# Performance work log

Measured on AMD Instinct MI355X. Metric: run time of the kernel, lower is better.

Reference implementation:

```python
import jax, jax.numpy as jnp
import numpy as np
import itertools

SEQ, NF, K, SD, NB, NC, NOBJ = 8, 4, 3, 256, 512, 174, 10
BELTA, SUB, BATCH = 0.1, 10, 256
SCALES = list(range(NF, 0, -1))  # [4, 3, 2, 1]
D = (K + 1) * SD                 # per-frame fused feature dim = 1024


def _adjust_scales(seq_ind, is_test):
    # mirrors adjust_scale_train / adjust_scale_test
    scale_max = NF * 2
    if seq_ind < scale_max:
        return SCALES[-seq_ind:] if is_test else SCALES[-min(SUB, seq_ind):]
    return SCALES[:min(SUB, seq_ind) + 1]


def _plan(is_test):
    # Static (non-traced) relation-index plan: for each seq_ind, the set of
    # arithmetic-progression frame combinations selected by select_idx().
    plan = []
    for seq_ind in range(1, SEQ + 1):
        entries = []
        for scale in _adjust_scales(seq_ind, is_test):
            k = min(scale, seq_ind)
            division = seq_ind // scale
            sel = [r for r in itertools.combinations(range(seq_ind), k)
                   if np.all(np.diff(np.asarray(r)) == division)]
            if sel:
                entries.append((scale, np.asarray(sel, dtype=np.int32)))
        plan.append(entries)
    return plan


def _temporal_variation(init_input):
    # VLAD-style soft residuals. Source runs kmeans (non-deterministic,
    # numpy/detached); we use deterministic centers = first K points per clip
    # and reproduce the exact downstream math, including the (buggy but
    # faithful) scalar spectral-norm soft assignment shared by all points.
    x = init_input.reshape(-1, SEQ, NOBJ, SD)              # (B, S, O, d)
    flat = x.reshape(x.shape[0], SEQ * NOBJ, SD)           # (B, N, d)
    centers = flat[:, :K, :]                               # (B, K, d)
    diff = flat[:, None, :, :] - centers[:, :, None, :]    # (B, K, N, d)
    sig = jnp.linalg.svd(diff, compute_uv=False)[..., 0]   # matrix 2-norm per (b, k)
    w = jax.nn.softmax(-BELTA * sig ** 2, axis=-1)         # (B, K), same for every point
    # S[b,t,k,:] = sum_o w[b,k] * (x[b,t,o,:] - c[b,k,:])
    var = w[:, None, :, None] * (x.sum(axis=2)[:, :, None, :] - NOBJ * centers[:, None, :, :])
    return jax.lax.stop_gradient(var)  # source detaches via .detach().numpy()


def _fusion(x, w1, b1, w2, b2):
    # Sequential(ReLU, Linear, ReLU, Linear)
    h = jnp.maximum(jax.nn.relu(x) @ w1 + b1, 0.0)
    return h @ w2 + b2


def _forward(graph_out, init_input, params, is_test):
    B = graph_out.shape[0]
    var = _temporal_variation(init_input)                      # (B, S, K, d)
    new_input = jnp.concatenate([var.reshape(B, SEQ, K * SD), graph_out], axis=2)  # (B, S, D)
    rows = []
    for entries in _plan(bool(is_test)):
        acc = jnp.zeros((B, NC), graph_out.dtype)
        for scale, rel in entries:
            # batched gather of all sampled relations at once: (B, R, scale, D)
            g = new_input[:, rel, :].reshape(B, rel.shape[0], scale * D)
            acc = acc + _fusion(g, *params[scale]).sum(axis=1)
        rows.append(acc)
    return jnp.stack(rows, axis=1).reshape(B * SEQ, NC)


def setup_inputs():
    key = jax.random.key(0)
    ks = jax.random.split(key, 2 + 2 * len(SCALES))
    inp = {
        "graph_out": jax.random.normal(ks[0], (BATCH, SEQ, SD), jnp.float32),
        "init_input": jax.random.normal(ks[1], (BATCH * SEQ, NOBJ, SD), jnp.float32),
        "is_test": 0,
    }
    for i, s in enumerate(SCALES):
        inp[f"w1_{s}"] = jax.random.normal(ks[2 + 2 * i], (s * D, NB), jnp.float32) * 0.02
        inp[f"b1_{s}"] = jnp.zeros((NB,), jnp.float32)
        inp[f"w2_{s}"] = jax.random.normal(ks[3 + 2 * i], (NB, NC), jnp.float32) * 0.02
        inp[f"b2_{s}"] = jnp.zeros((NC,), jnp.float32)
    return inp


def reference(graph_out, init_input, is_test, w1_4, b1_4, w2_4, b2_4, w1_3, b1_3, w2_3, b2_3, w1_2, b1_2, w2_2, b2_2, w1_1, b1_1, w2_1, b2_1):
    params = {4: (w1_4, b1_4, w2_4, b2_4), 3: (w1_3, b1_3, w2_3, b2_3),
              2: (w1_2, b1_2, w2_2, b2_2), 1: (w1_1, b1_1, w2_1, b2_1)}
    return _forward(graph_out, init_input, params, is_test)
```

## Files before the change

kernel.cpp:

```cpp
#include <hip/hip_runtime.h>
#include <math.h>
#include <stdint.h>


typedef __attribute__((ext_vector_type(8))) short short8v;
typedef __attribute__((ext_vector_type(4))) short short4v;
typedef __attribute__((ext_vector_type(4))) float f32x4;

__device__ __forceinline__ short f2bf(float f) {
  uint32_t u = __float_as_uint(f);
  u += 0x7fffu + ((u >> 16) & 1u);
  return (short)(u >> 16);
}
__device__ __forceinline__ float bf2f(short s) {
  return __uint_as_float(((uint32_t)(uint16_t)s) << 16);
}
__device__ __forceinline__ void gload16(const void* g, void* l) {
  __builtin_amdgcn_global_load_lds(
      (const __attribute__((address_space(1))) void*)g,
      (__attribute__((address_space(3))) void*)l, 16, 0, 0);
}

__device__ const int8_t ROWS4[12][5] = {
  {3, 0,1,2,3},
  {4, 0,1,2,3},{4, 1,2,3,4},
  {5, 0,1,2,3},{5, 1,2,3,4},{5, 2,3,4,5},
  {6, 0,1,2,3},{6, 1,2,3,4},{6, 2,3,4,5},{6, 3,4,5,6},
  {7, 0,2,4,6},{7, 1,3,5,7},
};
__device__ const int8_t ROWS3[15][4] = {
  {2, 0,1,2},
  {3, 0,1,2},{3, 1,2,3},
  {4, 0,1,2},{4, 1,2,3},{4, 2,3,4},
  {5, 0,2,4},{5, 1,3,5},
  {6, 0,2,4},{6, 1,3,5},{6, 2,4,6},
  {7, 0,2,4},{7, 1,3,5},{7, 2,4,6},{7, 3,5,7},
};
__device__ const int8_t ROWS2[19][3] = {
  {1, 0,1},
  {2, 0,1},{2, 1,2},
  {3, 0,2},{3, 1,3},
  {4, 0,2},{4, 1,3},{4, 2,4},
  {5, 0,3},{5, 1,4},{5, 2,5},
  {6, 0,3},{6, 1,4},{6, 2,5},{6, 3,6},
  {7, 0,4},{7, 1,5},{7, 2,6},{7, 3,7},
};
__device__ const int8_t ROWS1[36][2] = {
  {0,0},
  {1,0},{1,1},
  {2,0},{2,1},{2,2},
  {3,0},{3,1},{3,2},{3,3},
  {4,0},{4,1},{4,2},{4,3},{4,4},
  {5,0},{5,1},{5,2},{5,3},{5,4},{5,5},
  {6,0},{6,1},{6,2},{6,3},{6,4},{6,5},{6,6},
  {7,0},{7,1},{7,2},{7,3},{7,4},{7,5},{7,6},{7,7},
};
__device__ const float CNT[8][4] = {
  {0,0,0,1},{0,0,1,2},{0,1,2,3},{1,2,2,4},
  {2,3,3,5},{3,2,3,6},{4,3,4,7},{2,4,4,8},
};

#define OFF_S     42240
#define OFF_XSUM  68480
#define OFF_VBUF  76672
#define OFF_PBUF  78688
#define OFF_UU    80608
#define OFF_SCAL  81568
#define SMEM_SZ   81664

__global__ __launch_bounds__(512, 4) void fused_var_prep(
    const float* __restrict__ init, const float* __restrict__ graph,
    const float* __restrict__ w1_4, const float* __restrict__ w1_3,
    const float* __restrict__ w1_2, const float* __restrict__ w1_1,
    const float* __restrict__ w2a, const float* __restrict__ w2b,
    const float* __restrict__ w2c, const float* __restrict__ w2d,
    short* __restrict__ Rbuf, short* __restrict__ W1T, short* __restrict__ W2T)
{
  __shared__ __align__(16) char smem[SMEM_SZ];
  const int tid = threadIdx.x;
  const int blk = blockIdx.x;

  if (blk >= 256) {
    if (blk < 1536) {
      float* sh = (float*)smem;
      const int pb = blk - 256;
      const int slice = pb >> 7;
      const int rem = pb & 127;
      const int k0 = (rem & 15) * 64, c0 = (rem >> 4) * 64;
      const float* W1; int j;
      if (slice < 4)      { W1 = w1_4; j = slice; }
      else if (slice < 7) { W1 = w1_3; j = slice - 4; }
      else if (slice < 9) { W1 = w1_2; j = slice - 7; }
      else                { W1 = w1_1; j = 0; }
#pragma unroll
      for (int q = tid; q < 1024; q += 512) {
        int r = q >> 4, cq = (q & 15) * 4;
        f32x4 v = *(const f32x4*)(W1 + (size_t)(j * 1024 + k0 + r) * 512 + c0 + cq);
        *(f32x4*)&sh[r * 68 + cq] = v;
      }
      __syncthreads();
#pragma unroll
      for (int q = tid; q < 1024; q += 512) {
        int cc = q >> 4, kq = (q & 15) * 4;
        short4v sv;
#pragma unroll
        for (int m = 0; m < 4; ++m) sv[m] = f2bf(sh[(kq + m) * 68 + cc]);
        *(short4v*)&W1T[(size_t)(slice * 512 + c0 + cc) * 1024 + k0 + kq] = sv;
      }
    } else {
      int idx = (blk - 1536) * 2048 + tid * 4;
      int col = idx >> 11, kg = idx & 2047;
      int si = kg >> 9, kr = kg & 511;
      const float* w = (si == 0) ? w2a : (si == 1) ? w2b : (si == 2) ? w2c : w2d;
      short4v sv;
#pragma unroll
      for (int q = 0; q < 4; ++q)
        sv[q] = (col < 174) ? f2bf(w[(size_t)(kr + q) * 174 + col]) : (short)0;
      *(short4v*)&W2T[idx] = sv;
    }
    return;
  }

  float* bigf = (float*)smem;
  f32x4* big4 = (f32x4*)smem;
  float* Sm   = (float*)(smem + OFF_S);
  float* xsm  = (float*)(smem + OFF_XSUM);
  float* vb   = (float*)(smem + OFF_VBUF);
  float* pb   = (float*)(smem + OFF_PBUF);
  float* uum  = (float*)(smem + OFF_UU);
  float* scal = (float*)(smem + OFF_SCAL);

  const int b = blk;
  const float* fb = init + (size_t)b * 80 * 256;

  int g_ti = 0, g_tj = 0, g_h = -1;
  if (tid < 380) {
    int p = tid >> 1; g_h = tid & 1;
    int ti = 0, rem = p;
    while (rem >= 19 - ti) { rem -= 19 - ti; ++ti; }
    g_ti = ti; g_tj = ti + 1 + rem;
  } else if (tid < 400) {
    g_ti = g_tj = tid - 380;
  }

  float acc[4][4];
#pragma unroll
  for (int r = 0; r < 4; ++r)
#pragma unroll
    for (int c = 0; c < 4; ++c) acc[r][c] = 0.f;

  for (int ch = 0; ch < 2; ++ch) {
    __syncthreads();
#pragma unroll
    for (int q = tid; q < 2560; q += 512) {
      int r = q >> 5, c4 = q & 31;
      f32x4 v = *(const f32x4*)(fb + (size_t)r * 256 + ch * 128 + c4 * 4);
      big4[r * 33 + (c4 ^ ((r >> 2) & 7))] = v;
    }
    __syncthreads();
    if (tid < 400) {
      const int i0 = g_ti * 4, j0 = g_tj * 4;
      const int swzA = g_ti & 7, swzB = g_tj & 7;
      const int q0 = (g_h == 1) ? 16 : 0;
      const int qn = (g_h == -1) ? 32 : 16;
      if (g_h == -1) {
        for (int q = q0; q < q0 + qn; ++q) {
          f32x4 a[4];
#pragma unroll
          for (int r = 0; r < 4; ++r) a[r] = big4[(i0 + r) * 33 + (q ^ swzA)];
#pragma unroll
          for (int r = 0; r < 4; ++r)
#pragma unroll
            for (int c = 0; c < 4; ++c)
              acc[r][c] += a[r].x * a[c].x + a[r].y * a[c].y +
                           a[r].z * a[c].z + a[r].w * a[c].w;
        }
      } else {
        for (int q = q0; q < q0 + qn; ++q) {
          f32x4 a[4], bb[4];
#pragma unroll
          for (int r = 0; r < 4; ++r) a[r]  = big4[(i0 + r) * 33 + (q ^ swzA)];
#pragma unroll
          for (int c = 0; c < 4; ++c) bb[c] = big4[(j0 + c) * 33 + (q ^ swzB)];
#pragma unroll
          for (int r = 0; r < 4; ++r)
#pragma unroll
            for (int c = 0; c < 4; ++c)
              acc[r][c] += a[r].x * bb[c].x + a[r].y * bb[c].y +
                           a[r].z * bb[c].z + a[r].w * bb[c].w;
        }
      }
    } else if (tid >= 400) {
      const int idx = tid - 400;
      for (int p = idx; p < 1024; p += 112) {
        int t = p >> 7, d = p & 127;
        float s = 0.f;
#pragma unroll
        for (int o = 0; o < 10; ++o) {
          int row = t * 10 + o;
          s += bigf[row * 132 + (((d >> 2) ^ ((row >> 2) & 7)) << 2) + (d & 3)];
        }
        xsm[t * 256 + ch * 128 + d] = s;
      }
    }
  }
  __syncthreads();

  if (tid < 380) {
    const int i0 = g_ti * 4, j0 = g_tj * 4;
    if (g_h == 0) {
#pragma unroll
      for (int r = 0; r < 4; ++r)
#pragma unroll
        for (int c = 0; c < 4; ++c) Sm[(i0 + r) * 82 + j0 + c] = acc[r][c];
    } else {
#pragma unroll
      for (int r = 0; r < 4; ++r)
#pragma unroll
        for (int c = 0; c < 4; ++c) Sm[(j0 + c) * 82 + i0 + r] = acc[r][c];
    }
  } else if (tid < 400) {
    const int i0 = g_ti * 4;
#pragma unroll
    for (int r = 0; r < 4; ++r)
#pragma unroll
      for (int c = 0; c < 4; ++c) Sm[(i0 + r) * 82 + i0 + c] = acc[r][c];
  }
  __syncthreads();

  for (int e = tid; e < 3040; e += 512) {
    int p = e >> 4, rc = e & 15;
    int ti = 0, rem = p;
    while (rem >= 19 - ti) { rem -= 19 - ti; ++ti; }
    int tj = ti + 1 + rem;
    int i = ti * 4 + (rc >> 2), j = tj * 4 + (rc & 3);
    float s = Sm[i * 82 + j] + Sm[j * 82 + i];
    Sm[i * 82 + j] = s;
    Sm[j * 82 + i] = s;
  }
  if (tid < 240) vb[(0 * 3 + tid / 80) * 84 + (tid - (tid / 80) * 80)] = 1.0f;
  __syncthreads();

  int cur = 0;
  for (int it = 0; it < 5; ++it) {
    const bool last = (it == 4);
    if (tid < 480) {
      const int k = tid / 160, rem = tid - k * 160;
      const int h = rem / 80, i = rem - h * 80;
      const float* Si = Sm + i * 82 + h * 40;
      const float* vk = vb + (cur * 3 + k) * 84 + h * 40;
      float p = 0.f;
#pragma unroll
      for (int q = 0; q < 20; ++q) {
        float2 aa = *(const float2*)(Si + q * 2);
        float2 vv = *(const float2*)(vk + q * 2);
        p += aa.x * vv.x + aa.y * vv.y;
      }
      pb[tid] = p;
    } else if (tid < 486) {
      const int w = tid - 480;
      const int k = (w < 3) ? w : w - 3;
      const float* vk = vb + (cur * 3 + k) * 84;
      float s = 0.f;
      if (w < 3) {
        for (int j2 = 0; j2 < 80; ++j2) s += vk[j2];
        scal[k] = s;
      } else {
        const float* Sk = Sm + k * 82;
        for (int j2 = 0; j2 < 80; ++j2) s += Sk[j2] * vk[j2];
        scal[3 + k] = s;
      }
    }
    __syncthreads();
    if (tid < 240) {
      const int k = tid / 80, i = tid - k * 80;
      const float sg = scal[k], tu = scal[3 + k];
      float u = pb[k * 160 + i] + pb[k * 160 + 80 + i]
              - Sm[i * 82 + k] * sg - tu + Sm[k * 82 + k] * sg;
      if (!last) vb[((cur ^ 1) * 3 + k) * 84 + i] = u * 6.103515625e-05f;
      else       uum[k * 80 + i] = u;
    }
    __syncthreads();
    if (!last) cur ^= 1;
  }

  if (tid < 192) {
    const int k = tid >> 6, lane = tid & 63;
    float v1 = vb[(cur * 3 + k) * 84 + lane];
    float u1 = uum[k * 80 + lane];
    float a = u1 * v1, b2 = v1 * v1;
    if (lane < 16) {
      float v2 = vb[(cur * 3 + k) * 84 + 64 + lane];
      float u2 = uum[k * 80 + 64 + lane];
      a += u2 * v2; b2 += v2 * v2;
    }
#pragma unroll
    for (int m = 32; m >= 1; m >>= 1) {
      a += __shfl_xor(a, m);
      b2 += __shfl_xor(b2, m);
    }
    if (lane == 0) scal[9 + k] = a / b2;
  }
  __syncthreads();
  if (tid == 0) {
    float L0 = -0.1f * scal[9], L1 = -0.1f * scal[10], L2 = -0.1f * scal[11];
    float m = fmaxf(L0, fmaxf(L1, L2));
    float e0 = expf(L0 - m), e1 = expf(L1 - m), e2 = expf(L2 - m);
    float inv = 1.0f / (e0 + e1 + e2);
    scal[6] = e0 * inv; scal[7] = e1 * inv; scal[8] = e2 * inv;
  }
  __syncthreads();

  {
    const int t = tid >> 6, d0 = (tid & 63) * 4;
    const float w0 = scal[6], w1 = scal[7], w2 = scal[8];
    f32x4 xs = *(const f32x4*)(xsm + t * 256 + d0);
    f32x4 c0 = *(const f32x4*)(fb + 0 * 256 + d0);
    f32x4 c1 = *(const f32x4*)(fb + 1 * 256 + d0);
    f32x4 c2 = *(const f32x4*)(fb + 2 * 256 + d0);
    f32x4 go = *(const f32x4*)(graph + (size_t)(b * 8 + t) * 256 + d0);
    size_t rb = ((size_t)(b * 8 + t)) * 1024;
    short4v s0, s1, s2, s3;
#pragma unroll
    for (int q = 0; q < 4; ++q) {
      float xq = xs[q];
      s0[q] = f2bf(fmaxf(w0 * (xq - 10.f * c0[q]), 0.f));
      s1[q] = f2bf(fmaxf(w1 * (xq - 10.f * c1[q]), 0.f));
      s2[q] = f2bf(fmaxf(w2 * (xq - 10.f * c2[q]), 0.f));
      s3[q] = f2bf(fmaxf(go[q], 0.f));
    }
    *(short4v*)&Rbuf[rb + 0 + d0]   = s0;
    *(short4v*)&Rbuf[rb + 256 + d0] = s1;
    *(short4v*)&Rbuf[rb + 512 + d0] = s2;
    *(short4v*)&Rbuf[rb + 768 + d0] = s3;
  }
}

__global__ __launch_bounds__(256) void p_mfma(
    const short* __restrict__ A, const short* __restrict__ W1T,
    short* __restrict__ P)
{
  __shared__ short As[128 * 32];
  __shared__ short Bs[128 * 32];
  const int id = blockIdx.x + blockIdx.y * 40;
  const int nid = (id & 7) * 80 + (id >> 3);
  const int bx = nid >> 4, by = nid & 15;
  const int tid = threadIdx.x, lane = tid & 63, w = tid >> 6;
  const int wr = w >> 1, wc = w & 1;
  const int rowBase = by * 128;
  const short* Bp = W1T + (size_t)bx * 128 * 1024;
  const int rA = w * 16 + (lane >> 2);
  const int kkA = (lane & 3) * 8;

  f32x4 acc[4][4];
#pragma unroll
  for (int m = 0; m < 4; ++m)
#pragma unroll
    for (int n = 0; n < 4; ++n) acc[m][n] = (f32x4){0.f, 0.f, 0.f, 0.f};

  for (int k0 = 0; k0 < 1024; k0 += 32) {
    __syncthreads();
    gload16(A + (size_t)(rowBase + rA) * 1024 + k0 + kkA, As + w * 512);
    gload16(A + (size_t)(rowBase + 64 + rA) * 1024 + k0 + kkA, As + 2048 + w * 512);
    gload16(Bp + (size_t)rA * 1024 + k0 + kkA, Bs + w * 512);
    gload16(Bp + (size_t)(64 + rA) * 1024 + k0 + kkA, Bs + 2048 + w * 512);
    __syncthreads();
    short8v a[4], bv[4];
#pragma unroll
    for (int m = 0; m < 4; ++m)
      a[m] = *(const short8v*)(As + (wr * 64 + m * 16 + (lane & 15)) * 32 + (lane >> 4) * 8);
#pragma unroll
    for (int n = 0; n < 4; ++n)
      bv[n] = *(const short8v*)(Bs + (wc * 64 + n * 16 + (lane & 15)) * 32 + (lane >> 4) * 8);
#pragma unroll
    for (int m = 0; m < 4; ++m)
#pragma unroll
      for (int n = 0; n < 4; ++n)
        acc[m][n] = __builtin_amdgcn_mfma_f32_16x16x32_bf16(a[m], bv[n], acc[m][n], 0, 0, 0);
  }

  const int colG = bx * 128 + wc * 64;
#pragma unroll
  for (int m = 0; m < 4; ++m) {
    int row = rowBase + wr * 64 + m * 16 + (lane >> 4) * 4;
#pragma unroll
    for (int n = 0; n < 4; ++n) {
      int col = colG + n * 16 + (lane & 15);
#pragma unroll
      for (int r = 0; r < 4; ++r)
        P[(size_t)(row + r) * 5120 + col] = f2bf(acc[m][n][r]);
    }
  }
}

__global__ __launch_bounds__(256) void hsum_all(
    const short* __restrict__ P,
    const float* __restrict__ b1a, const float* __restrict__ b1b,
    const float* __restrict__ b1c, const float* __restrict__ b1d,
    short* __restrict__ Hsum)
{
  const int row = blockIdx.x, t = row & 7, base = row - t;
  const int c0 = threadIdx.x * 2;
  const size_t prow = (size_t)base * 5120;

  {
    float2 bb = *(const float2*)(b1a + c0);
    float a0 = 0.f, a1 = 0.f;
    for (int r = 0; r < 12; ++r) {
      if (ROWS4[r][0] != t) continue;
      float h0 = bb.x, h1 = bb.y;
#pragma unroll
      for (int jj = 0; jj < 4; ++jj) {
        const short2 pv = *(const short2*)(P + prow + (size_t)ROWS4[r][1 + jj] * 5120 + jj * 512 + c0);
        h0 += bf2f(pv.x); h1 += bf2f(pv.y);
      }
      a0 += fmaxf(h0, 0.f); a1 += fmaxf(h1, 0.f);
    }
    uint32_t wv = (uint32_t)(uint16_t)f2bf(a0) | ((uint32_t)(uint16_t)f2bf(a1) << 16);
    *(uint32_t*)&Hsum[(size_t)row * 2048 + c0] = wv;
  }
  {
    float2 bb = *(const float2*)(b1b + c0);
    float a0 = 0.f, a1 = 0.f;
    for (int r = 0; r < 15; ++r) {
      if (ROWS3[r][0] != t) continue;
      float h0 = bb.x, h1 = bb.y;
#pragma unroll
      for (int jj = 0; jj < 3; ++jj) {
        const short2 pv = *(const short2*)(P + prow + (size_t)ROWS3[r][1 + jj] * 5120 + 2048 + jj * 512 + c0);
        h0 += bf2f(pv.x); h1 += bf2f(pv.y);
      }
      a0 += fmaxf(h0, 0.f); a1 += fmaxf(h1, 0.f);
    }
    uint32_t wv = (uint32_t)(uint16_t)f2bf(a0) | ((uint32_t)(uint16_t)f2bf(a1) << 16);
    *(uint32_t*)&Hsum[(size_t)row * 2048 + 512 + c0] = wv;
  }
  {
    float2 bb = *(const float2*)(b1c + c0);
    float a0 = 0.f, a1 = 0.f;
    for (int r = 0; r < 19; ++r) {
      if (ROWS2[r][0] != t) continue;
      float h0 = bb.x, h1 = bb.y;
#pragma unroll
      for (int jj = 0; jj < 2; ++jj) {
        const short2 pv = *(const short2*)(P + prow + (size_t)ROWS2[r][1 + jj] * 5120 + 3584 + jj * 512 + c0);
        h0 += bf2f(pv.x); h1 += bf2f(pv.y);
      }
      a0 += fmaxf(h0, 0.f); a1 += fmaxf(h1, 0.f);
    }
    uint32_t wv = (uint32_t)(uint16_t)f2bf(a0) | ((uint32_t)(uint16_t)f2bf(a1) << 16);
    *(uint32_t*)&Hsum[(size_t)row * 2048 + 1024 + c0] = wv;
  }
  {
    float2 bb = *(const float2*)(b1d + c0);
    float a0 = 0.f, a1 = 0.f;
    for (int r = 0; r < 36; ++r) {
      if (ROWS1[r][0] != t) continue;
      const short2 pv = *(const short2*)(P + prow + (size_t)ROWS1[r][1] * 5120 + 4608 + c0);
      a0 += fmaxf(bb.x + bf2f(pv.x), 0.f);
      a1 += fmaxf(bb.y + bf2f(pv.y), 0.f);
    }
    uint32_t wv = (uint32_t)(uint16_t)f2bf(a0) | ((uint32_t)(uint16_t)f2bf(a1) << 16);
    *(uint32_t*)&Hsum[(size_t)row * 2048 + 1536 + c0] = wv;
  }
}

__global__ __launch_bounds__(256) void out_split(
    const short* __restrict__ H, const short* __restrict__ W2T,
    float* __restrict__ partial)
{
  __shared__ short As[128 * 32];
  __shared__ short Bs[64 * 32];
  const int tid = threadIdx.x, lane = tid & 63, w = tid >> 6;
  const int wr = w >> 1, wc = w & 1;
  const int rowBase = blockIdx.y * 128, colBase = blockIdx.x * 64;
  const int kBase = blockIdx.z * 512;
  const int rA = w * 16 + (lane >> 2);
  const int kkA = (lane & 3) * 8;

  f32x4 acc[4][2];
#pragma unroll
  for (int m = 0; m < 4; ++m)
#pragma unroll
    for (int n = 0; n < 2; ++n) acc[m][n] = (f32x4){0.f, 0.f, 0.f, 0.f};

  for (int k0 = 0; k0 < 512; k0 += 32) {
    const int kg = kBase + k0;
    __syncthreads();
    gload16(H + (size_t)(rowBase + rA) * 2048 + kg + kkA, As + w * 512);
    gload16(H + (size_t)(rowBase + 64 + rA) * 2048 + kg + kkA, As + 2048 + w * 512);
    gload16(W2T + (size_t)(colBase + rA) * 2048 + kg + kkA, Bs + w * 512);
    __syncthreads();
    short8v a[4], bv[2];
#pragma unroll
    for (int m = 0; m < 4; ++m)
      a[m] = *(const short8v*)(As + (wr * 64 + m * 16 + (lane & 15)) * 32 + (lane >> 4) * 8);
#pragma unroll
    for (int n = 0; n < 2; ++n)
      bv[n] = *(const short8v*)(Bs + (wc * 32 + n * 16 + (lane & 15)) * 32 + (lane >> 4) * 8);
#pragma unroll
    for (int m = 0; m < 4; ++m)
#pragma unroll
      for (int n = 0; n < 2; ++n)
        acc[m][n] = __builtin_amdgcn_mfma_f32_16x16x32_bf16(a[m], bv[n], acc[m][n], 0, 0, 0);
  }

  float* pz = partial + (size_t)blockIdx.z * 2048 * 192;
#pragma unroll
  for (int n = 0; n < 2; ++n) {
    int col = colBase + wc * 32 + n * 16 + (lane & 15);
#pragma unroll
    for (int m = 0; m < 4; ++m) {
      int row0 = rowBase + wr * 64 + m * 16 + (lane >> 4) * 4;
#pragma unroll
      for (int r = 0; r < 4; ++r)
        pz[(size_t)(row0 + r) * 192 + col] = acc[m][n][r];
    }
  }
}

__global__ __launch_bounds__(256) void out_reduce(
    const float* __restrict__ partial,
    const float* __restrict__ b2a, const float* __restrict__ b2b,
    const float* __restrict__ b2c, const float* __restrict__ b2d,
    float* __restrict__ out)
{
  const int row = blockIdx.x, col = threadIdx.x;
  if (col >= 174) return;
  const size_t o = (size_t)row * 192 + col;
  float s = partial[o] + partial[o + (size_t)2048 * 192]
          + partial[o + (size_t)4096 * 192] + partial[o + (size_t)6144 * 192];
  int tt = row & 7;
  float bias = CNT[tt][0] * b2a[col] + CNT[tt][1] * b2b[col]
             + CNT[tt][2] * b2c[col] + CNT[tt][3] * b2d[col];
  out[(size_t)row * 174 + col] = s + bias;
}

extern "C" void kernel_launch(void* const* d_in, const int* in_sizes, int n_in,
                              void* d_out, int out_size, void* d_ws, size_t ws_size,
                              hipStream_t stream) {
  const float* graph = (const float*)d_in[0];
  const float* init  = (const float*)d_in[1];
  const float* w1[4] = {(const float*)d_in[3],  (const float*)d_in[7],
                        (const float*)d_in[11], (const float*)d_in[15]};
  const float* b1[4] = {(const float*)d_in[4],  (const float*)d_in[8],
                        (const float*)d_in[12], (const float*)d_in[16]};
  const float* w2[4] = {(const float*)d_in[5],  (const float*)d_in[9],
                        (const float*)d_in[13], (const float*)d_in[17]};
  const float* b2[4] = {(const float*)d_in[6],  (const float*)d_in[10],
                        (const float*)d_in[14], (const float*)d_in[18]};
  float* out = (float*)d_out;

  char* ws = (char*)d_ws;
  short* Rbf  = (short*)(ws + 0);
  short* W1T  = (short*)(ws + ((size_t)4  << 20));
  short* P    = (short*)(ws + ((size_t)14 << 20));
  short* W2T  = (short*)(ws + ((size_t)34 << 20));
  short* Hsum = (short*)(ws + 0);
  float* Part = (float*)(ws + ((size_t)8 << 20));

  fused_var_prep<<<1728, 512, 0, stream>>>(init, graph,
                                           w1[0], w1[1], w1[2], w1[3],
                                           w2[0], w2[1], w2[2], w2[3],
                                           Rbf, W1T, W2T);

  p_mfma<<<dim3(40, 16), 256, 0, stream>>>(Rbf, W1T, P);

  hsum_all<<<2048, 256, 0, stream>>>(P, b1[0], b1[1], b1[2], b1[3], Hsum);

  out_split<<<dim3(3, 16, 4), 256, 0, stream>>>(Hsum, W2T, Part);

  out_reduce<<<2048, 256, 0, stream>>>(Part, b2[0], b2[1], b2[2], b2[3], out);
}
```

Before: 107.3 us.

## Compute per-clip Gram matrix with split-bf16 MFMA and split weight prep kernel

The 80x80 Gram matrix per clip moves from scalar FP32 dot products to MFMA 16x16x32 bf16 instructions. Precision is kept near FP32 by splitting each value into high and low bf16 parts and summing three cross products. The object-sum reduction is fused into the load/convert pass, and the power-iteration matvec is reorganised to one thread per output using full symmetric rows. Weight transposition/conversion moves into a separate kernel, which adds a launch but lets the Gram kernel run at 256 threads with a smaller footprint. The bf16 split may change numerics slightly compared to the FP32 path.

Measured after the change: 94.45 us (median of 2 runs). 1.14x faster.

```diff
diff --git a/kernel.cpp b/kernel.cpp
--- a/kernel.cpp
+++ b/kernel.cpp
@@ -60,238 +60,154 @@
   {2,3,3,5},{3,2,3,6},{4,3,4,7},{2,4,4,8},
 };
 
-#define OFF_S     42240
-#define OFF_XSUM  68480
-#define OFF_VBUF  76672
-#define OFF_PBUF  78688
-#define OFF_UU    80608
-#define OFF_SCAL  81568
-#define SMEM_SZ   81664
-
-__global__ __launch_bounds__(512, 4) void fused_var_prep(
+#define GV_FH    0
+#define GV_FL    20480
+#define GV_S     40960
+#define GV_XSUM  67840
+#define GV_VB    76032
+#define GV_UU    78048
+#define GV_SCAL  79008
+#define GV_SZ    79056
+
+__global__ __launch_bounds__(256) void gram_var(
     const float* __restrict__ init, const float* __restrict__ graph,
-    const float* __restrict__ w1_4, const float* __restrict__ w1_3,
-    const float* __restrict__ w1_2, const float* __restrict__ w1_1,
-    const float* __restrict__ w2a, const float* __restrict__ w2b,
-    const float* __restrict__ w2c, const float* __restrict__ w2d,
-    short* __restrict__ Rbuf, short* __restrict__ W1T, short* __restrict__ W2T)
+    short* __restrict__ Rbuf)
 {
-  __shared__ __align__(16) char smem[SMEM_SZ];
-  const int tid = threadIdx.x;
-  const int blk = blockIdx.x;
-
-  if (blk >= 256) {
-    if (blk < 1536) {
-      float* sh = (float*)smem;
-      const int pb = blk - 256;
-      const int slice = pb >> 7;
-      const int rem = pb & 127;
-      const int k0 = (rem & 15) * 64, c0 = (rem >> 4) * 64;
-      const float* W1; int j;
-      if (slice < 4)      { W1 = w1_4; j = slice; }
-      else if (slice < 7) { W1 = w1_3; j = slice - 4; }
-      else if (slice < 9) { W1 = w1_2; j = slice - 7; }
-      else                { W1 = w1_1; j = 0; }
-#pragma unroll
-      for (int q = tid; q < 1024; q += 512) {
-        int r = q >> 4, cq = (q & 15) * 4;
-        f32x4 v = *(const f32x4*)(W1 + (size_t)(j * 1024 + k0 + r) * 512 + c0 + cq);
-        *(f32x4*)&sh[r * 68 + cq] = v;
-      }
-      __syncthreads();
-#pragma unroll
-      for (int q = tid; q < 1024; q += 512) {
-        int cc = q >> 4, kq = (q & 15) * 4;
-        short4v sv;
-#pragma unroll
-        for (int m = 0; m < 4; ++m) sv[m] = f2bf(sh[(kq + m) * 68 + cc]);
-        *(short4v*)&W1T[(size_t)(slice * 512 + c0 + cc) * 1024 + k0 + kq] = sv;
-      }
-    } else {
-      int idx = (blk - 1536) * 2048 + tid * 4;
-      int col = idx >> 11, kg = idx & 2047;
-      int si = kg >> 9, kr = kg & 511;
-      const float* w = (si == 0) ? w2a : (si == 1) ? w2b : (si == 2) ? w2c : w2d;
-      short4v sv;
-#pragma unroll
-      for (int q = 0; q < 4; ++q)
-        sv[q] = (col < 174) ? f2bf(w[(size_t)(kr + q) * 174 + col]) : (short)0;
-      *(short4v*)&W2T[idx] = sv;
-    }
-    return;
-  }
-
-  float* bigf = (float*)smem;
-  f32x4* big4 = (f32x4*)smem;
-  float* Sm   = (float*)(smem + OFF_S);
-  float* xsm  = (float*)(smem + OFF_XSUM);
-  float* vb   = (float*)(smem + OFF_VBUF);
-  float* pb   = (float*)(smem + OFF_PBUF);
-  float* uum  = (float*)(smem + OFF_UU);
-  float* scal = (float*)(smem + OFF_SCAL);
-
-  const int b = blk;
+  __shared__ __align__(16) char smem[GV_SZ];
+  short* Fh  = (short*)(smem + GV_FH);
+  short* Fl  = (short*)(smem + GV_FL);
+  float* Sm  = (float*)(smem + GV_S);
+  float* xsm = (float*)(smem + GV_XSUM);
+  float* vb  = (float*)(smem + GV_VB);
+  float* uum = (float*)(smem + GV_UU);
+  float* scal= (float*)(smem + GV_SCAL);
+
+  const int tid = threadIdx.x, lane = tid & 63, w = tid >> 6;
+  const int b = blockIdx.x;
   const float* fb = init + (size_t)b * 80 * 256;
 
-  int g_ti = 0, g_tj = 0, g_h = -1;
-  if (tid < 380) {
-    int p = tid >> 1; g_h = tid & 1;
-    int ti = 0, rem = p;
-    while (rem >= 19 - ti) { rem -= 19 - ti; ++ti; }
-    g_ti = ti; g_tj = ti + 1 + rem;
-  } else if (tid < 400) {
-    g_ti = g_tj = tid - 380;
-  }
-
-  float acc[4][4];
-#pragma unroll
-  for (int r = 0; r < 4; ++r)
-#pragma unroll
-    for (int c = 0; c < 4; ++c) acc[r][c] = 0.f;
+  int ti_[7], tj_[7];
+#pragma unroll
+  for (int q = 0; q < 7; ++q) {
+    int tt = w + q * 4;
+    int t5 = (tt < 25) ? tt : 0;
+    ti_[q] = t5 / 5; tj_[q] = t5 % 5;
+  }
+
+  f32x4 acc[7];
+#pragma unroll
+  for (int q = 0; q < 7; ++q) acc[q] = (f32x4){0.f, 0.f, 0.f, 0.f};
 
   for (int ch = 0; ch < 2; ++ch) {
     __syncthreads();
-#pragma unroll
-    for (int q = tid; q < 2560; q += 512) {
-      int r = q >> 5, c4 = q & 31;
-      f32x4 v = *(const f32x4*)(fb + (size_t)r * 256 + ch * 128 + c4 * 4);
-      big4[r * 33 + (c4 ^ ((r >> 2) & 7))] = v;
-    }
-    __syncthreads();
-    if (tid < 400) {
-      const int i0 = g_ti * 4, j0 = g_tj * 4;
-      const int swzA = g_ti & 7, swzB = g_tj & 7;
-      const int q0 = (g_h == 1) ? 16 : 0;
-      const int qn = (g_h == -1) ? 32 : 16;
-      if (g_h == -1) {
-        for (int q = q0; q < q0 + qn; ++q) {
-          f32x4 a[4];
-#pragma unroll
-          for (int r = 0; r < 4; ++r) a[r] = big4[(i0 + r) * 33 + (q ^ swzA)];
-#pragma unroll
-          for (int r = 0; r < 4; ++r)
-#pragma unroll
-            for (int c = 0; c < 4; ++c)
-              acc[r][c] += a[r].x * a[c].x + a[r].y * a[c].y +
-                           a[r].z * a[c].z + a[r].w * a[c].w;
+    {
+      const int t = tid >> 5, kq = tid & 31;
+      const float* src = fb + (size_t)(t * 10) * 256 + ch * 128 + kq * 4;
+      f32x4 sum = (f32x4){0.f, 0.f, 0.f, 0.f};
+#pragma unroll
+      for (int o = 0; o < 10; ++o) {
+        f32x4 v = *(const f32x4*)(src + (size_t)o * 256);
+        int r = t * 10 + o;
+        int byte8 = r * 256 + ((kq * 8) ^ ((r & 7) << 4));
+        short4v hv, lv;
+#pragma unroll
+        for (int e = 0; e < 4; ++e) {
+          short h = f2bf(v[e]);
+          hv[e] = h;
+          lv[e] = f2bf(v[e] - bf2f(h));
         }
-      } else {
-        for (int q = q0; q < q0 + qn; ++q) {
-          f32x4 a[4], bb[4];
-#pragma unroll
-          for (int r = 0; r < 4; ++r) a[r]  = big4[(i0 + r) * 33 + (q ^ swzA)];
-#pragma unroll
-          for (int c = 0; c < 4; ++c) bb[c] = big4[(j0 + c) * 33 + (q ^ swzB)];
-#pragma unroll
-          for (int r = 0; r < 4; ++r)
-#pragma unroll
-            for (int c = 0; c < 4; ++c)
-              acc[r][c] += a[r].x * bb[c].x + a[r].y * bb[c].y +
-                           a[r].z * bb[c].z + a[r].w * bb[c].w;
+        *(short4v*)((char*)Fh + byte8) = hv;
+        *(short4v*)((char*)Fl + byte8) = lv;
+        sum += v;
+      }
+      *(f32x4*)(xsm + t * 256 + ch * 128 + kq * 4) = sum;
+    }
+    __syncthreads();
+
+#pragma unroll
+    for (int ks = 0; ks < 4; ++ks) {
+      const int koff2 = (ks * 32 + (lane >> 4) * 8) * 2;
+#pragma unroll
+      for (int q = 0; q < 7; ++q) {
+        const int tt = w + q * 4;
+        if (tt < 25) {
+          int ra = ti_[q] * 16 + (lane & 15);
+          int rb = tj_[q] * 16 + (lane & 15);
+          int ba = ra * 256 + (koff2 ^ ((ra & 7) << 4));
+          int bb = rb * 256 + (koff2 ^ ((rb & 7) << 4));
+          short8v ah = *(const short8v*)((char*)Fh + ba);
+          short8v al = *(const short8v*)((char*)Fl + ba);
+          short8v bh = *(const short8v*)((char*)Fh + bb);
+          short8v bl = *(const short8v*)((char*)Fl + bb);
+          acc[q] = __builtin_amdgcn_mfma_f32_16x16x32_bf16(ah, bh, acc[q], 0, 0, 0);
+          acc[q] = __builtin_amdgcn_mfma_f32_16x16x32_bf16(ah, bl, acc[q], 0, 0, 0);
+          acc[q] = __builtin_amdgcn_mfma_f32_16x16x32_bf16(al, bh, acc[q], 0, 0, 0);
         }
       }
-    } else if (tid >= 400) {
-      const int idx = tid - 400;
-      for (int p = idx; p < 1024; p += 112) {
-        int t = p >> 7, d = p & 127;
-        float s = 0.f;
-#pragma unroll
-        for (int o = 0; o < 10; ++o) {
-          int row = t * 10 + o;
-          s += bigf[row * 132 + (((d >> 2) ^ ((row >> 2) & 7)) << 2) + (d & 3)];
-        }
-        xsm[t * 256 + ch * 128 + d] = s;
-      }
-    }
-  }
+    }
+  }
+
+#pragma unroll
+  for (int q = 0; q < 7; ++q) {
+    const int tt = w + q * 4;
+    if (tt < 25) {
+      int row0 = ti_[q] * 16 + (lane >> 4) * 4;
+      int col = tj_[q] * 16 + (lane & 15);
+#pragma unroll
+      for (int r = 0; r < 4; ++r) Sm[(row0 + r) * 84 + col] = acc[q][r];
+    }
+  }
+  if (tid < 240) vb[(0 * 3 + tid / 80) * 84 + (tid % 80)] = 1.0f;
   __syncthreads();
 
-  if (tid < 380) {
-    const int i0 = g_ti * 4, j0 = g_tj * 4;
-    if (g_h == 0) {
-#pragma unroll
-      for (int r = 0; r < 4; ++r)
-#pragma unroll
-        for (int c = 0; c < 4; ++c) Sm[(i0 + r) * 82 + j0 + c] = acc[r][c];
-    } else {
-#pragma unroll
-      for (int r = 0; r < 4; ++r)
-#pragma unroll
-        for (int c = 0; c < 4; ++c) Sm[(j0 + c) * 82 + i0 + r] = acc[r][c];
-    }
-  } else if (tid < 400) {
-    const int i0 = g_ti * 4;
-#pragma unroll
-    for (int r = 0; r < 4; ++r)
-#pragma unroll
-      for (int c = 0; c < 4; ++c) Sm[(i0 + r) * 82 + i0 + c] = acc[r][c];
-  }
-  __syncthreads();
-
-  for (int e = tid; e < 3040; e += 512) {
-    int p = e >> 4, rc = e & 15;
-    int ti = 0, rem = p;
-    while (rem >= 19 - ti) { rem -= 19 - ti; ++ti; }
-    int tj = ti + 1 + rem;
-    int i = ti * 4 + (rc >> 2), j = tj * 4 + (rc & 3);
-    float s = Sm[i * 82 + j] + Sm[j * 82 + i];
-    Sm[i * 82 + j] = s;
-    Sm[j * 82 + i] = s;
-  }
-  if (tid < 240) vb[(0 * 3 + tid / 80) * 84 + (tid - (tid / 80) * 80)] = 1.0f;
-  __syncthreads();
-
+  const int pk = (tid < 240) ? tid / 80 : 0;
+  const int pi = (tid < 240) ? tid % 80 : 0;
   int cur = 0;
   for (int it = 0; it < 5; ++it) {
     const bool last = (it == 4);
-    if (tid < 480) {
-      const int k = tid / 160, rem = tid - k * 160;
-      const int h = rem / 80, i = rem - h * 80;
-      const float* Si = Sm + i * 82 + h * 40;
-      const float* vk = vb + (cur * 3 + k) * 84 + h * 40;
-      float p = 0.f;
-#pragma unroll
-      for (int q = 0; q < 20; ++q) {
-        float2 aa = *(const float2*)(Si + q * 2);
-        float2 vv = *(const float2*)(vk + q * 2);
-        p += aa.x * vv.x + aa.y * vv.y;
-      }
-      pb[tid] = p;
-    } else if (tid < 486) {
-      const int w = tid - 480;
-      const int k = (w < 3) ? w : w - 3;
+    float u = 0.f;
+    if (tid < 240) {
+      const float* Si = Sm + pi * 84;
+      const float* vk = vb + (cur * 3 + pk) * 84;
+#pragma unroll
+      for (int q2 = 0; q2 < 20; ++q2) {
+        f32x4 aa = *(const f32x4*)(Si + q2 * 4);
+        f32x4 vv = *(const f32x4*)(vk + q2 * 4);
+        u += aa.x * vv.x + aa.y * vv.y + aa.z * vv.z + aa.w * vv.w;
+      }
+    } else if (tid < 246) {
+      int w2 = tid - 240;
+      int k = (w2 < 3) ? w2 : w2 - 3;
       const float* vk = vb + (cur * 3 + k) * 84;
       float s = 0.f;
-      if (w < 3) {
+      if (w2 < 3) {
         for (int j2 = 0; j2 < 80; ++j2) s += vk[j2];
         scal[k] = s;
       } else {
-        const float* Sk = Sm + k * 82;
+        const float* Sk = Sm + k * 84;
         for (int j2 = 0; j2 < 80; ++j2) s += Sk[j2] * vk[j2];
         scal[3 + k] = s;
       }
     }
     __syncthreads();
     if (tid < 240) {
-      const int k = tid / 80, i = tid - k * 80;
-      const float sg = scal[k], tu = scal[3 + k];
-      float u = pb[k * 160 + i] + pb[k * 160 + 80 + i]
-              - Sm[i * 82 + k] * sg - tu + Sm[k * 82 + k] * sg;
-      if (!last) vb[((cur ^ 1) * 3 + k) * 84 + i] = u * 6.103515625e-05f;
-      else       uum[k * 80 + i] = u;
+      float sg = scal[pk], tu = scal[3 + pk];
+      float un = u - Sm[pi * 84 + pk] * sg - tu + Sm[pk * 84 + pk] * sg;
+      if (!last) vb[((cur ^ 1) * 3 + pk) * 84 + pi] = un * 6.103515625e-05f;
+      else       uum[pk * 80 + pi] = un;
     }
     __syncthreads();
     if (!last) cur ^= 1;
   }
 
   if (tid < 192) {
-    const int k = tid >> 6, lane = tid & 63;
-    float v1 = vb[(cur * 3 + k) * 84 + lane];
-    float u1 = uum[k * 80 + lane];
+    const int k = tid >> 6, ln = tid & 63;
+    float v1 = vb[(cur * 3 + k) * 84 + ln];
+    float u1 = uum[k * 80 + ln];
     float a = u1 * v1, b2 = v1 * v1;
-    if (lane < 16) {
-      float v2 = vb[(cur * 3 + k) * 84 + 64 + lane];
-      float u2 = uum[k * 80 + 64 + lane];
+    if (ln < 16) {
+      float v2 = vb[(cur * 3 + k) * 84 + 64 + ln];
+      float u2 = uum[k * 80 + 64 + ln];
       a += u2 * v2; b2 += v2 * v2;
     }
 #pragma unroll
@@ -299,7 +215,7 @@
       a += __shfl_xor(a, m);
       b2 += __shfl_xor(b2, m);
     }
-    if (lane == 0) scal[9 + k] = a / b2;
+    if (ln == 0) scal[9 + k] = a / b2;
   }
   __syncthreads();
   if (tid == 0) {
@@ -312,27 +228,77 @@
   __syncthreads();
 
   {
-    const int t = tid >> 6, d0 = (tid & 63) * 4;
     const float w0 = scal[6], w1 = scal[7], w2 = scal[8];
-    f32x4 xs = *(const f32x4*)(xsm + t * 256 + d0);
-    f32x4 c0 = *(const f32x4*)(fb + 0 * 256 + d0);
-    f32x4 c1 = *(const f32x4*)(fb + 1 * 256 + d0);
-    f32x4 c2 = *(const f32x4*)(fb + 2 * 256 + d0);
-    f32x4 go = *(const f32x4*)(graph + (size_t)(b * 8 + t) * 256 + d0);
-    size_t rb = ((size_t)(b * 8 + t)) * 1024;
-    short4v s0, s1, s2, s3;
-#pragma unroll
-    for (int q = 0; q < 4; ++q) {
-      float xq = xs[q];
-      s0[q] = f2bf(fmaxf(w0 * (xq - 10.f * c0[q]), 0.f));
-      s1[q] = f2bf(fmaxf(w1 * (xq - 10.f * c1[q]), 0.f));
-      s2[q] = f2bf(fmaxf(w2 * (xq - 10.f * c2[q]), 0.f));
-      s3[q] = f2bf(fmaxf(go[q], 0.f));
-    }
-    *(short4v*)&Rbuf[rb + 0 + d0]   = s0;
-    *(short4v*)&Rbuf[rb + 256 + d0] = s1;
-    *(short4v*)&Rbuf[rb + 512 + d0] = s2;
-    *(short4v*)&Rbuf[rb + 768 + d0] = s3;
+    const int d0 = (tid & 63) * 4;
+#pragma unroll
+    for (int p = 0; p < 2; ++p) {
+      const int t = p * 4 + (tid >> 6);
+      f32x4 xs = *(const f32x4*)(xsm + t * 256 + d0);
+      f32x4 c0 = *(const f32x4*)(fb + 0 * 256 + d0);
+      f32x4 c1 = *(const f32x4*)(fb + 1 * 256 + d0);
+      f32x4 c2 = *(const f32x4*)(fb + 2 * 256 + d0);
+      f32x4 go = *(const f32x4*)(graph + (size_t)(b * 8 + t) * 256 + d0);
+      size_t rb = ((size_t)(b * 8 + t)) * 1024;
+      short4v s0, s1, s2, s3;
+#pragma unroll
+      for (int q = 0; q < 4; ++q) {
+        float xq = xs[q];
+        s0[q] = f2bf(fmaxf(w0 * (xq - 10.f * c0[q]), 0.f));
+        s1[q] = f2bf(fmaxf(w1 * (xq - 10.f * c1[q]), 0.f));
+        s2[q] = f2bf(fmaxf(w2 * (xq - 10.f * c2[q]), 0.f));
+        s3[q] = f2bf(fmaxf(go[q], 0.f));
+      }
+      *(short4v*)&Rbuf[rb + 0 + d0]   = s0;
+      *(short4v*)&Rbuf[rb + 256 + d0] = s1;
+      *(short4v*)&Rbuf[rb + 512 + d0] = s2;
+      *(short4v*)&Rbuf[rb + 768 + d0] = s3;
+    }
+  }
+}
+
+__global__ __launch_bounds__(512) void prep_weights(
+    const float* __restrict__ w1_4, const float* __restrict__ w1_3,
+    const float* __restrict__ w1_2, const float* __restrict__ w1_1,
+    const float* __restrict__ w2a, const float* __restrict__ w2b,
+    const float* __restrict__ w2c, const float* __restrict__ w2d,
+    short* __restrict__ W1T, short* __restrict__ W2T)
+{
+  __shared__ float sh[64 * 65];
+  const int blk = blockIdx.x, tid = threadIdx.x;
+  if (blk < 1280) {
+    const int slice = blk >> 7, rem = blk & 127;
+    const int k0 = (rem & 15) * 64, c0 = (rem >> 4) * 64;
+    const float* W1; int j;
+    if (slice < 4)      { W1 = w1_4; j = slice; }
+    else if (slice < 7) { W1 = w1_3; j = slice - 4; }
+    else if (slice < 9) { W1 = w1_2; j = slice - 7; }
+    else                { W1 = w1_1; j = 0; }
+#pragma unroll
+    for (int q = tid; q < 1024; q += 512) {
+      int r = q >> 4, cq = (q & 15) * 4;
+      f32x4 v = *(const f32x4*)(W1 + (size_t)(j * 1024 + k0 + r) * 512 + c0 + cq);
+      sh[r * 65 + cq + 0] = v.x; sh[r * 65 + cq + 1] = v.y;
+      sh[r * 65 + cq + 2] = v.z; sh[r * 65 + cq + 3] = v.w;
+    }
+    __syncthreads();
+#pragma unroll
+    for (int q = tid; q < 1024; q += 512) {
+      int cc = q >> 4, kq = (q & 15) * 4;
+      short4v sv;
+#pragma unroll
+      for (int m = 0; m < 4; ++m) sv[m] = f2bf(sh[(kq + m) * 65 + cc]);
+      *(short4v*)&W1T[(size_t)(slice * 512 + c0 + cc) * 1024 + k0 + kq] = sv;
+    }
+  } else {
+    int idx = (blk - 1280) * 2048 + tid * 4;
+    int col = idx >> 11, kg = idx & 2047;
+    int si = kg >> 9, kr = kg & 511;
+    const float* w = (si == 0) ? w2a : (si == 1) ? w2b : (si == 2) ? w2c : w2d;
+    short4v sv;
+#pragma unroll
+    for (int q = 0; q < 4; ++q)
+      sv[q] = (col < 174) ? f2bf(w[(size_t)(kr + q) * 174 + col]) : (short)0;
+    *(short4v*)&W2T[idx] = sv;
   }
 }
 
@@ -559,10 +525,10 @@
   short* Hsum = (short*)(ws + 0);
   float* Part = (float*)(ws + ((size_t)8 << 20));
 
-  fused_var_prep<<<1728, 512, 0, stream>>>(init, graph,
-                                           w1[0], w1[1], w1[2], w1[3],
-                                           w2[0], w2[1], w2[2], w2[3],
-                                           Rbf, W1T, W2T);
+  gram_var<<<256, 256, 0, stream>>>(init, graph, Rbf);
+
+  prep_weights<<<1472, 512, 0, stream>>>(w1[0], w1[1], w1[2], w1[3],
+                                         w2[0], w2[1], w2[2], w2[3], W1T, W2T);
 
   p_mfma<<<dim3(40, 16), 256, 0, stream>>>(Rbf, W1T, P);
 
```
